# Kernel tuning notes

Hardware: AMD Instinct MI355X
Metric: run time of the kernel (lower is better)

## Reference

```python
import jax, jax.numpy as jnp
import numpy as np

NY = NX = 256
NT = 256
B = 2
NSRC = 2
NREC = 64
DY = DX = 5.0
DT = 5e-4
PML = 20
PML_FREQ = 25.0


def setup_inputs() -> dict:
    key = jax.random.key(0)
    k1, k2, k3, k4, k5, k6 = jax.random.split(key, 6)
    # physically plausible elastic model
    vp = 3000.0 + 200.0 * jax.random.uniform(k1, (NY, NX), dtype=jnp.float32)
    vs = 1500.0 + 100.0 * jax.random.uniform(k2, (NY, NX), dtype=jnp.float32)
    rho = 2200.0 + 100.0 * jax.random.uniform(k3, (NY, NX), dtype=jnp.float32)
    lamb = rho * (vp ** 2 - 2.0 * vs ** 2)
    mu = rho * vs ** 2
    buoyancy = 1.0 / rho
    source_amplitudes_y = 1e3 * jax.random.normal(k4, (B, NSRC, NT), dtype=jnp.float32)
    lo, hi = PML + 10, NY - PML - 10  # keep sources/receivers inside the PML
    source_locations_y = jax.random.randint(k5, (B, NSRC, 2), lo, hi)
    receiver_locations_y = jax.random.randint(k6, (B, NREC, 2), lo, hi)
    return {
        "lamb": lamb,
        "mu": mu,
        "buoyancy": buoyancy,
        "source_amplitudes_y": source_amplitudes_y,
        "source_locations_y": source_locations_y,
        "receiver_locations_y": receiver_locations_y,
    }


def _pml_coeffs(n, width, dx, dt, max_vel, freq):
    # C-PML coefficients a, b along one axis; zero outside the PML region.
    i = jnp.arange(n, dtype=jnp.float32)
    frac = jnp.maximum(
        jnp.clip((width - i) / width, 0.0, 1.0),
        jnp.clip((i - (n - 1 - width)) / width, 0.0, 1.0),
    )
    sigma_max = 3.0 * max_vel * np.log(1000.0) / (2.0 * width * dx)
    sigma = sigma_max * frac ** 2
    alpha = np.pi * freq * (1.0 - frac)
    b = jnp.exp(-(sigma + alpha) * dt)
    a = sigma / (sigma + alpha + 1e-9) * (b - 1.0)
    return a, b


# staggered 2nd-order forward/backward differences (zero beyond the edge)
def _dfy(f):
    return jnp.pad(f[:, 1:] - f[:, :-1], ((0, 0), (0, 1), (0, 0))) / DY

def _dby(f):
    return jnp.pad(f[:, 1:] - f[:, :-1], ((0, 0), (1, 0), (0, 0))) / DY

def _dfx(f):
    return jnp.pad(f[:, :, 1:] - f[:, :, :-1], ((0, 0), (0, 0), (0, 1))) / DX

def _dbx(f):
    return jnp.pad(f[:, :, 1:] - f[:, :, :-1], ((0, 0), (0, 0), (1, 0))) / DX


def _forward(lamb, mu, buoyancy, amps, src_loc, rec_loc):
    ny, nx = lamb.shape
    bsz, nsrc, nt = amps.shape
    max_vel = jax.lax.stop_gradient(jnp.sqrt((lamb + 2.0 * mu) * buoyancy).max())
    ay, by = _pml_coeffs(ny, PML, DY, DT, max_vel, PML_FREQ)
    ax, bx = _pml_coeffs(nx, PML, DX, DT, max_vel, PML_FREQ)
    ay, by = ay[None, :, None], by[None, :, None]
    ax, bx = ax[None, None, :], bx[None, None, :]
    sb = jnp.arange(bsz)[:, None]
    sy, sx = src_loc[..., 0], src_loc[..., 1]
    ry, rx = rec_loc[..., 0], rec_loc[..., 1]
    src_scale = DT * buoyancy[sy, sx]  # [B, nsrc]
    l2m = lamb + 2.0 * mu
    z = jnp.zeros((bsz, ny, nx), lamb.dtype)
    fields0 = (z,) * 13  # vy, vx, syy, sxy, sxx + 8 PML memory fields

    def step(carry, amp_t):
        (vy, vx, syy, sxy, sxx,
         m_syyy, m_sxyx, m_sxyy, m_sxxx,
         m_vyy, m_vxx, m_vyx, m_vxy) = carry
        # velocity updates (with PML memory on stress derivatives)
        d = _dby(syy); m_syyy = by * m_syyy + ay * d; d_syy_y = d + m_syyy
        d = _dbx(sxy); m_sxyx = bx * m_sxyx + ax * d; d_sxy_x = d + m_sxyx
        vy = vy + DT * buoyancy * (d_syy_y + d_sxy_x)
        d = _dfy(sxy); m_sxyy = by * m_sxyy + ay * d; d_sxy_y = d + m_sxyy
        d = _dfx(sxx); m_sxxx = bx * m_sxxx + ax * d; d_sxx_x = d + m_sxxx
        vx = vx + DT * buoyancy * (d_sxy_y + d_sxx_x)
        # y-oriented source injection into vy
        vy = vy.at[sb, sy, sx].add(amp_t * src_scale)
        # stress updates (with PML memory on velocity derivatives)
        d = _dfy(vy); m_vyy = by * m_vyy + ay * d; d_vy_y = d + m_vyy
        d = _dbx(vx); m_vxx = bx * m_vxx + ax * d; d_vx_x = d + m_vxx
        syy = syy + DT * (l2m * d_vy_y + lamb * d_vx_x)
        sxx = sxx + DT * (lamb * d_vy_y + l2m * d_vx_x)
        d = _dbx(vy); m_vyx = bx * m_vyx + ax * d; d_vy_x = d + m_vyx
        d = _dby(vx); m_vxy = by * m_vxy + ay * d; d_vx_y = d + m_vxy
        sxy = sxy + DT * mu * (d_vy_x + d_vx_y)
        rec = vy[sb, ry, rx]  # [B, nrec]
        return (vy, vx, syy, sxy, sxx,
                m_syyy, m_sxyx, m_sxyy, m_sxxx,
                m_vyy, m_vxx, m_vyx, m_vxy), rec

    _, recs = jax.lax.scan(jax.checkpoint(step), fields0, jnp.transpose(amps, (2, 0, 1)))
    return jnp.transpose(recs, (1, 2, 0))  # [shot, receiver, time]


def reference(lamb, mu, buoyancy, source_amplitudes_y, source_locations_y, receiver_locations_y):
    return _forward(lamb, mu, buoyancy, source_amplitudes_y,
                    source_locations_y, receiver_locations_y)
```

## Files before the change

### kernel.cpp

```cpp
#include <hip/hip_runtime.h>

#define NXc 256
#define NTc 256
#define NBLK 128
#define DTv 0.0005f
#define INVD 0.2f

#define COEF_OFF 0
#define EX_OFF  1024
#define EX_BLK  2048

__device__ __forceinline__ unsigned long long tld(const unsigned long long* p) {
  return __hip_atomic_load(p, __ATOMIC_RELAXED, __HIP_MEMORY_SCOPE_AGENT);
}
__device__ __forceinline__ void tst(unsigned long long* p, float v, unsigned tag) {
  unsigned long long u = ((unsigned long long)tag << 32) | (unsigned long long)__float_as_uint(v);
  __hip_atomic_store(p, u, __ATOMIC_RELAXED, __HIP_MEMORY_SCOPE_AGENT);
}
#define TVAL(x) __uint_as_float((unsigned)(x))
#define TTAG(x) ((unsigned)((x) >> 32))

__device__ __forceinline__ void bar_lds() {
  asm volatile("s_waitcnt lgkmcnt(0)" ::: "memory");
  __builtin_amdgcn_s_barrier();
  asm volatile("" ::: "memory");
}

__global__ __launch_bounds__(256) void setup_kernel(
    const float* __restrict__ lamb, const float* __restrict__ mu,
    const float* __restrict__ buoy, float* __restrict__ coef)
{
  __shared__ float red[256];
  const int tid = threadIdx.x;
  float m = 0.0f;
  for (int i = tid; i < 256*256; i += 256)
    m = fmaxf(m, sqrtf((lamb[i] + 2.0f*mu[i]) * buoy[i]));
  red[tid] = m;
  __syncthreads();
  for (int s = 128; s > 0; s >>= 1) {
    if (tid < s) red[tid] = fmaxf(red[tid], red[tid+s]);
    __syncthreads();
  }
  const float maxv = red[0];
  const float i_f = (float)tid;
  const float w = 20.0f;
  float f1 = fminf(fmaxf((w - i_f) * (1.0f/w), 0.0f), 1.0f);
  float f2 = fminf(fmaxf((i_f - (256.0f - 1.0f - w)) * (1.0f/w), 0.0f), 1.0f);
  float frac = fmaxf(f1, f2);
  float sigma_max = 3.0f * maxv * 6.907755278982137f / (2.0f * w * 5.0f);
  float sigma = sigma_max * frac * frac;
  float alpha = 3.14159265358979323f * 25.0f * (1.0f - frac);
  float bc = expf(-(sigma + alpha) * 0.0005f);
  float ac = sigma / (sigma + alpha + 1e-9f) * (bc - 1.0f);
  coef[tid]       = ac;
  coef[256 + tid] = bc;
  coef[512 + tid] = ac;
  coef[768 + tid] = bc;
}

__global__ __launch_bounds__(256) void elastic_col(
    const float* __restrict__ lamb_g, const float* __restrict__ mu_g,
    const float* __restrict__ buoy_g, const float* __restrict__ amps,
    const int* __restrict__ src_loc, const int* __restrict__ rec_loc,
    float* __restrict__ ws, float* __restrict__ out)
{
  __shared__ float SxyB[4][6], SxxB[4][6], VyB[4][4], VxB[4][4];

  const int blk = blockIdx.x;
  const int b = blk >> 6, bi = blk & 63;
  const int tx = threadIdx.x;
  const int lane = tx & 63, wv = tx >> 6;
  const int lo = bi << 2;
  const bool hasUp = bi > 0, hasDn = bi < 63;
  const bool xm_ok = tx > 0, xp_ok = tx < 255;

  const float* coef = ws + COEF_OFF;
  unsigned long long* exb = (unsigned long long*)(ws + EX_OFF);

  const float axv = coef[512+tx], bxv = coef[768+tx];

  float vy[6], vx[6], myy[6], myx[6], mxyy[6], mxx[6];
  float cay[6], cby[6], vdtb[6];
  #pragma unroll
  for (int r = 0; r < 6; ++r) {
    const int gy = lo - 1 + r;
    const bool ok = (gy >= 0) && (gy < 256);
    const int gc = ok ? gy : 0;
    vdtb[r] = ok ? DTv * buoy_g[gc*NXc + tx] : 0.f;
    cay[r]  = ok ? coef[gc] : 0.f;
    cby[r]  = ok ? coef[256+gc] : 1.f;
    vy[r]=vx[r]=myy[r]=myx[r]=mxyy[r]=mxx[r]=0.f;
  }
  float syy[4], sxy[4], sxx[4], mvyy[4], mvxx[4], mvyx[4], mvxy[4];
  float slam[4], smu[4], sl2m[4];
  #pragma unroll
  for (int j = 0; j < 4; ++j) {
    const int gy = lo + j;
    slam[j] = lamb_g[gy*NXc+tx]; smu[j] = mu_g[gy*NXc+tx];
    sl2m[j] = slam[j] + 2.f*smu[j];
    syy[j]=sxy[j]=sxx[j]=mvyy[j]=mvxx[j]=mvyx[j]=mvxy[j]=0.f;
  }

  int sk0=-1, sk1=-1, so0=0, so1=0;
  for (int i = 0; i < 4; ++i) {
    const int sb = i >> 1, sy = src_loc[2*i], sx = src_loc[2*i+1];
    if (sb == b && sx == tx) {
      const int r = sy - (lo - 1);
      if (r >= 0 && r < 6) { if (sk0 < 0) { sk0=r; so0=i*NTc; } else { sk1=r; so1=i*NTc; } }
    }
  }
  unsigned long long rL0=0,rH0=0,rL1=0,rH1=0,rL2=0,rH2=0,rL3=0,rH3=0;
  for (int i = 0; i < 128; ++i) {
    const int rb = i >> 6, ry = rec_loc[2*i], rx = rec_loc[2*i+1];
    if (rb == b && rx == tx) {
      const unsigned long long bit = 1ull << (i & 63);
      if (ry == lo)   { if (i<64) rL0|=bit; else rH0|=bit; }
      if (ry == lo+1) { if (i<64) rL1|=bit; else rH1|=bit; }
      if (ry == lo+2) { if (i<64) rL2|=bit; else rH2|=bit; }
      if (ry == lo+3) { if (i<64) rL3|=bit; else rH3|=bit; }
    }
  }
  const bool anyrec = (rL0|rH0|rL1|rH1|rL2|rH2|rL3|rH3) != 0ull;

  if (tx < 4*6) { SxyB[tx/6][tx%6]=0.f; SxxB[tx/6][tx%6]=0.f; }
  if (tx < 4*4) { VyB[tx/4][tx%4]=0.f;  VxB[tx/4][tx%4]=0.f; }
  __syncthreads();

  for (int t = 0; t < NTc; ++t) {
    float a0=0.f, a1=0.f;
    if (sk0>=0) a0 = amps[so0+t];
    if (sk1>=0) a1 = amps[so1+t];

    unsigned long long uw0=0,uw1=0,uw2=0,uw3=0, dw0=0,dw1=0,dw2=0,dw3=0;
    if (t > 0) {
      const size_t ps = (size_t)((t-1)&1)*NBLK;
      const unsigned long long* up = exb + (ps + (hasUp?blk-1:blk))*EX_BLK + tx;
      const unsigned long long* dn = exb + (ps + (hasDn?blk+1:blk))*EX_BLK + tx;
      const unsigned want = (unsigned)t;
      for (;;) {
        if (hasUp) { uw0=tld(up+4*256); uw1=tld(up+5*256); uw2=tld(up+6*256); uw3=tld(up+7*256); }
        if (hasDn) { dw0=tld(dn+0*256); dw1=tld(dn+1*256); dw2=tld(dn+2*256); dw3=tld(dn+3*256); }
        bool ok = true;
        if (hasUp) ok = ok && TTAG(uw0)==want && TTAG(uw1)==want && TTAG(uw2)==want && TTAG(uw3)==want;
        if (hasDn) ok = ok && TTAG(dw0)==want && TTAG(dw1)==want && TTAG(dw2)==want && TTAG(dw3)==want;
        if (ok) break;
      }
    }
    const float syyU2=TVAL(uw0), syyU1=TVAL(uw1), sxyU1=TVAL(uw2), sxxU1=TVAL(uw3);
    const float syyD =TVAL(dw0), sxyD4=TVAL(dw1), sxyD5=TVAL(dw2), sxxD =TVAL(dw3);

    if (lane == 63) { SxyB[wv][0]=sxyU1; SxyB[wv][5]=sxyD4; }
    if (lane == 0)  { SxxB[wv][0]=sxxU1; SxxB[wv][5]=sxxD; }
    bar_lds();

    {
      const float syE[7]  = {syyU2, syyU1, syy[0],syy[1],syy[2],syy[3], syyD};
      const float sxyE[6] = {sxyU1, sxy[0],sxy[1],sxy[2],sxy[3], sxyD4};
      const float sxxE[6] = {sxxU1, sxx[0],sxx[1],sxx[2],sxx[3], sxxD};
      #pragma unroll
      for (int r = 0; r < 6; ++r) {
        float sxym = __shfl_up(sxyE[r], 1, 64);
        if (lane == 0 && wv > 0) sxym = SxyB[wv-1][r];
        float sxxp = __shfl_down(sxxE[r], 1, 64);
        if (lane == 63 && wv < 3) sxxp = SxxB[wv+1][r];
        if (r == 0 && !hasUp) continue;
        if (r == 5 && !hasDn) continue;
        const int gy = lo - 1 + r;
        float d, u1, u2, u3, u4;
        d = (gy > 0) ? (syE[r+1] - syE[r]) * INVD : 0.f;
        myy[r] = cby[r]*myy[r] + cay[r]*d; u1 = d + myy[r];
        d = xm_ok ? (sxyE[r] - sxym) * INVD : 0.f;
        myx[r] = bxv*myx[r] + axv*d; u2 = d + myx[r];
        vy[r] += vdtb[r]*(u1+u2);
        float dfy;
        if (r < 5) dfy = (gy < 255) ? (sxyE[r+1] - sxyE[r]) * INVD : 0.f;
        else       dfy = (sxyD5 - sxyD4) * INVD;
        mxyy[r] = cby[r]*mxyy[r] + cay[r]*dfy; u3 = dfy + mxyy[r];
        d = xp_ok ? (sxxp - sxxE[r]) * INVD : 0.f;
        mxx[r] = bxv*mxx[r] + axv*d; u4 = d + mxx[r];
        vx[r] += vdtb[r]*(u3+u4);
        if (r == sk0) vy[r] += a0*vdtb[r];
        if (r == sk1) vy[r] += a1*vdtb[r];
      }
    }
    if (lane == 63) {
      VyB[wv][0]=vy[1]; VyB[wv][1]=vy[2]; VyB[wv][2]=vy[3]; VyB[wv][3]=vy[4];
      VxB[wv][0]=vx[1]; VxB[wv][1]=vx[2]; VxB[wv][2]=vx[3]; VxB[wv][3]=vx[4];
    }
    bar_lds();

    if (anyrec) {
      unsigned long long m;
      m=rL0; while(m){int i=__ffsll((long long)m)-1;m&=m-1;out[i*NTc+t]=vy[1];}
      m=rH0; while(m){int i=__ffsll((long long)m)-1;m&=m-1;out[(i+64)*NTc+t]=vy[1];}
      m=rL1; while(m){int i=__ffsll((long long)m)-1;m&=m-1;out[i*NTc+t]=vy[2];}
      m=rH1; while(m){int i=__ffsll((long long)m)-1;m&=m-1;out[(i+64)*NTc+t]=vy[2];}
      m=rL2; while(m){int i=__ffsll((long long)m)-1;m&=m-1;out[i*NTc+t]=vy[3];}
      m=rH2; while(m){int i=__ffsll((long long)m)-1;m&=m-1;out[(i+64)*NTc+t]=vy[3];}
      m=rL3; while(m){int i=__ffsll((long long)m)-1;m&=m-1;out[i*NTc+t]=vy[4];}
      m=rH3; while(m){int i=__ffsll((long long)m)-1;m&=m-1;out[(i+64)*NTc+t]=vy[4];}
    }

    {
      float vym[4], vxm[4];
      #pragma unroll
      for (int j = 0; j < 4; ++j) {
        vym[j] = __shfl_up(vy[j+1], 1, 64);
        vxm[j] = __shfl_up(vx[j+1], 1, 64);
        if (lane == 0 && wv > 0) { vym[j] = VyB[wv-1][j]; vxm[j] = VxB[wv-1][j]; }
      }
      #pragma unroll
      for (int j = 0; j < 4; ++j) {
        const int gy = lo + j;
        float d, u5, u6, u7, u8;
        d = (gy < 255) ? (vy[j+2] - vy[j+1]) * INVD : 0.f;
        mvyy[j] = cby[j+1]*mvyy[j] + cay[j+1]*d; u5 = d + mvyy[j];
        d = xm_ok ? (vx[j+1] - vxm[j]) * INVD : 0.f;
        mvxx[j] = bxv*mvxx[j] + axv*d; u6 = d + mvxx[j];
        syy[j] += DTv*(sl2m[j]*u5 + slam[j]*u6);
        sxx[j] += DTv*(slam[j]*u5 + sl2m[j]*u6);
        d = xm_ok ? (vy[j+1] - vym[j]) * INVD : 0.f;
        mvyx[j] = bxv*mvyx[j] + axv*d; u7 = d + mvyx[j];
        d = (gy > 0) ? (vx[j+1] - vx[j]) * INVD : 0.f;
        mvxy[j] = cby[j+1]*mvxy[j] + cay[j+1]*d; u8 = d + mvxy[j];
        sxy[j] += DTv*smu[j]*(u7+u8);
      }
    }

    {
      unsigned long long* Q = exb + ((size_t)(t&1)*NBLK + blk)*EX_BLK + tx;
      const unsigned wt = (unsigned)(t+1);
      tst(Q+0*256, syy[0], wt); tst(Q+1*256, sxy[0], wt);
      tst(Q+2*256, sxy[1], wt); tst(Q+3*256, sxx[0], wt);
      tst(Q+4*256, syy[2], wt); tst(Q+5*256, syy[3], wt);
      tst(Q+6*256, sxy[3], wt); tst(Q+7*256, sxx[3], wt);
    }
    if (lane == 63) { SxyB[wv][1]=sxy[0]; SxyB[wv][2]=sxy[1]; SxyB[wv][3]=sxy[2]; SxyB[wv][4]=sxy[3]; }
    if (lane == 0)  { SxxB[wv][1]=sxx[0]; SxxB[wv][2]=sxx[1]; SxxB[wv][3]=sxx[2]; SxxB[wv][4]=sxx[3]; }
  }
}

extern "C" void kernel_launch(void* const* d_in, const int* in_sizes, int n_in,
                              void* d_out, int out_size, void* d_ws, size_t ws_size,
                              hipStream_t stream) {
  const float* lamb    = (const float*)d_in[0];
  const float* mu      = (const float*)d_in[1];
  const float* buoy    = (const float*)d_in[2];
  const float* amps    = (const float*)d_in[3];
  const int*   src_loc = (const int*)d_in[4];
  const int*   rec_loc = (const int*)d_in[5];
  float* out = (float*)d_out;
  float* ws  = (float*)d_ws;

  hipMemsetAsync((char*)ws + EX_OFF*sizeof(float), 0,
                 (size_t)2*NBLK*EX_BLK*sizeof(unsigned long long), stream);

  hipLaunchKernelGGL(setup_kernel, dim3(1), dim3(256), 0, stream,
                     lamb, mu, buoy, ws + COEF_OFF);

  void* args[] = { (void*)&lamb, (void*)&mu, (void*)&buoy, (void*)&amps,
                   (void*)&src_loc, (void*)&rec_loc, (void*)&ws, (void*)&out };
  hipLaunchCooperativeKernel((void*)elastic_col, dim3(NBLK), dim3(256),
                             args, 0, stream);
}
```

Measured before the change: 787.0 us.

## Split domain into 256 two-row blocks with full-stress halo exchange

Each block now owns 2 rows instead of 4, doubling the grid to 256 cooperative blocks so more CUs share the per-step serial work. Neighbours publish all six stress values per column, and each block recomputes the halo velocity rows itself from those values instead of receiving them. Edge lanes also read the adjacent column's halo entries directly from global memory. The cost is more flag-polling traffic per step and duplicated halo velocity work relative to the useful work per block.

```diff
diff --git a/kernel.cpp b/kernel.cpp
--- a/kernel.cpp
+++ b/kernel.cpp
@@ -2,13 +2,14 @@
 
 #define NXc 256
 #define NTc 256
-#define NBLK 128
+#define NBLK 256
 #define DTv 0.0005f
 #define INVD 0.2f
 
 #define COEF_OFF 0
 #define EX_OFF  1024
-#define EX_BLK  2048
+#define EX_ENT  6
+#define EX_BLK  (EX_ENT*256)
 
 __device__ __forceinline__ unsigned long long tld(const unsigned long long* p) {
   return __hip_atomic_load(p, __ATOMIC_RELAXED, __HIP_MEMORY_SCOPE_AGENT);
@@ -58,20 +59,20 @@
   coef[768 + tid] = bc;
 }
 
-__global__ __launch_bounds__(256) void elastic_col(
+__global__ __launch_bounds__(256) void elastic_n2(
     const float* __restrict__ lamb_g, const float* __restrict__ mu_g,
     const float* __restrict__ buoy_g, const float* __restrict__ amps,
     const int* __restrict__ src_loc, const int* __restrict__ rec_loc,
     float* __restrict__ ws, float* __restrict__ out)
 {
-  __shared__ float SxyB[4][6], SxxB[4][6], VyB[4][4], VxB[4][4];
+  __shared__ float SxyB[4][2], SxxB[4][2], VyB[4][2], VxB[4][2];
 
   const int blk = blockIdx.x;
-  const int b = blk >> 6, bi = blk & 63;
+  const int b = blk >> 7, n = blk & 127;
   const int tx = threadIdx.x;
   const int lane = tx & 63, wv = tx >> 6;
-  const int lo = bi << 2;
-  const bool hasUp = bi > 0, hasDn = bi < 63;
+  const int lo = n << 1;
+  const bool hasUp = n > 0, hasDn = n < 127;
   const bool xm_ok = tx > 0, xp_ok = tx < 255;
 
   const float* coef = ws + COEF_OFF;
@@ -79,51 +80,48 @@
 
   const float axv = coef[512+tx], bxv = coef[768+tx];
 
-  float vy[6], vx[6], myy[6], myx[6], mxyy[6], mxx[6];
-  float cay[6], cby[6], vdtb[6];
-  #pragma unroll
-  for (int r = 0; r < 6; ++r) {
-    const int gy = lo - 1 + r;
-    const bool ok = (gy >= 0) && (gy < 256);
-    const int gc = ok ? gy : 0;
-    vdtb[r] = ok ? DTv * buoy_g[gc*NXc + tx] : 0.f;
-    cay[r]  = ok ? coef[gc] : 0.f;
-    cby[r]  = ok ? coef[256+gc] : 1.f;
-    vy[r]=vx[r]=myy[r]=myx[r]=mxyy[r]=mxx[r]=0.f;
-  }
-  float syy[4], sxy[4], sxx[4], mvyy[4], mvxx[4], mvyx[4], mvxy[4];
-  float slam[4], smu[4], sl2m[4];
-  #pragma unroll
-  for (int j = 0; j < 4; ++j) {
-    const int gy = lo + j;
-    slam[j] = lamb_g[gy*NXc+tx]; smu[j] = mu_g[gy*NXc+tx];
-    sl2m[j] = slam[j] + 2.f*smu[j];
-    syy[j]=sxy[j]=sxx[j]=mvyy[j]=mvxx[j]=mvyx[j]=mvxy[j]=0.f;
-  }
+  const float ayU = hasUp ? coef[lo-1] : 0.f;
+  const float byU = hasUp ? coef[256+lo-1] : 1.f;
+  const float dtbU = hasUp ? DTv*buoy_g[(lo-1)*NXc+tx] : 0.f;
+  const float ay0 = coef[lo],   by0 = coef[256+lo];
+  const float dtb0 = DTv*buoy_g[lo*NXc+tx];
+  const float ay1 = coef[lo+1], by1 = coef[256+lo+1];
+  const float dtb1 = DTv*buoy_g[(lo+1)*NXc+tx];
+  const float ayD = hasDn ? coef[lo+2] : 0.f;
+  const float byD = hasDn ? coef[256+lo+2] : 1.f;
+  const float dtbD = hasDn ? DTv*buoy_g[(lo+2)*NXc+tx] : 0.f;
+  const float lam0 = lamb_g[lo*NXc+tx],     mu0 = mu_g[lo*NXc+tx],     l2m0 = lam0+2.f*mu0;
+  const float lam1 = lamb_g[(lo+1)*NXc+tx], mu1 = mu_g[(lo+1)*NXc+tx], l2m1 = lam1+2.f*mu1;
+
+  float vy0=0,vy1=0,vx0=0,vx1=0, vyU=0,vxU=0, vyD=0,vxD=0;
+  float myy0=0,myy1=0,myx0=0,myx1=0,mxyy0=0,mxyy1=0,mxx0=0,mxx1=0;
+  float myyU=0,myxU=0,mxyyU=0,mxxU=0, myyD=0,myxD=0,mxyyD=0,mxxD=0;
+  float syy0=0,syy1=0,sxy0=0,sxy1=0,sxx0=0,sxx1=0;
+  float mvyy0=0,mvyy1=0,mvxx0=0,mvxx1=0,mvyx0=0,mvyx1=0,mvxy0=0,mvxy1=0;
 
   int sk0=-1, sk1=-1, so0=0, so1=0;
   for (int i = 0; i < 4; ++i) {
     const int sb = i >> 1, sy = src_loc[2*i], sx = src_loc[2*i+1];
     if (sb == b && sx == tx) {
       const int r = sy - (lo - 1);
-      if (r >= 0 && r < 6) { if (sk0 < 0) { sk0=r; so0=i*NTc; } else { sk1=r; so1=i*NTc; } }
-    }
-  }
-  unsigned long long rL0=0,rH0=0,rL1=0,rH1=0,rL2=0,rH2=0,rL3=0,rH3=0;
+      if (r >= 0 && r < 4) { if (sk0 < 0) { sk0=r; so0=i*NTc; } else { sk1=r; so1=i*NTc; } }
+    }
+  }
+  unsigned long long rA0=0,rA1=0,rB0=0,rB1=0;
   for (int i = 0; i < 128; ++i) {
     const int rb = i >> 6, ry = rec_loc[2*i], rx = rec_loc[2*i+1];
     if (rb == b && rx == tx) {
       const unsigned long long bit = 1ull << (i & 63);
-      if (ry == lo)   { if (i<64) rL0|=bit; else rH0|=bit; }
-      if (ry == lo+1) { if (i<64) rL1|=bit; else rH1|=bit; }
-      if (ry == lo+2) { if (i<64) rL2|=bit; else rH2|=bit; }
-      if (ry == lo+3) { if (i<64) rL3|=bit; else rH3|=bit; }
-    }
-  }
-  const bool anyrec = (rL0|rH0|rL1|rH1|rL2|rH2|rL3|rH3) != 0ull;
-
-  if (tx < 4*6) { SxyB[tx/6][tx%6]=0.f; SxxB[tx/6][tx%6]=0.f; }
-  if (tx < 4*4) { VyB[tx/4][tx%4]=0.f;  VxB[tx/4][tx%4]=0.f; }
+      if (ry == lo)   { if (i<64) rA0|=bit; else rA1|=bit; }
+      if (ry == lo+1) { if (i<64) rB0|=bit; else rB1|=bit; }
+    }
+  }
+  const bool recA = (rA0|rA1)!=0ull, recB = (rB0|rB1)!=0ull;
+
+  if (tx < 8) {
+    SxyB[tx>>1][tx&1]=0.f; SxxB[tx>>1][tx&1]=0.f;
+    VyB[tx>>1][tx&1]=0.f;  VxB[tx>>1][tx&1]=0.f;
+  }
   __syncthreads();
 
   for (int t = 0; t < NTc; ++t) {
@@ -131,112 +129,154 @@
     if (sk0>=0) a0 = amps[so0+t];
     if (sk1>=0) a1 = amps[so1+t];
 
-    unsigned long long uw0=0,uw1=0,uw2=0,uw3=0, dw0=0,dw1=0,dw2=0,dw3=0;
-    if (t > 0) {
-      const size_t ps = (size_t)((t-1)&1)*NBLK;
-      const unsigned long long* up = exb + (ps + (hasUp?blk-1:blk))*EX_BLK + tx;
-      const unsigned long long* dn = exb + (ps + (hasDn?blk+1:blk))*EX_BLK + tx;
-      const unsigned want = (unsigned)t;
-      for (;;) {
-        if (hasUp) { uw0=tld(up+4*256); uw1=tld(up+5*256); uw2=tld(up+6*256); uw3=tld(up+7*256); }
-        if (hasDn) { dw0=tld(dn+0*256); dw1=tld(dn+1*256); dw2=tld(dn+2*256); dw3=tld(dn+3*256); }
-        bool ok = true;
-        if (hasUp) ok = ok && TTAG(uw0)==want && TTAG(uw1)==want && TTAG(uw2)==want && TTAG(uw3)==want;
-        if (hasDn) ok = ok && TTAG(dw0)==want && TTAG(dw1)==want && TTAG(dw2)==want && TTAG(dw3)==want;
-        if (ok) break;
+    const size_t ps = (size_t)((t+1)&1)*NBLK;
+    const unsigned long long* up = exb + (ps + (size_t)(hasUp?blk-1:blk))*EX_BLK + tx;
+    const unsigned long long* dn = exb + (ps + (size_t)(hasDn?blk+1:blk))*EX_BLK + tx;
+    const unsigned want = (unsigned)t;
+    unsigned long long u0=0,u1=0,u3=0,u5=0,u3m=0,u5p=0;
+    unsigned long long d0=0,d2=0,d3=0,d4=0,d2m=0,d4p=0;
+    for (;;) {
+      bool ok = true;
+      if (hasUp) {
+        u0=tld(up+0*256); u1=tld(up+1*256); u3=tld(up+3*256); u5=tld(up+5*256);
+        ok = ok && TTAG(u0)==want && TTAG(u1)==want && TTAG(u3)==want && TTAG(u5)==want;
+        if (lane==0 && xm_ok)  { u3m=tld(up+3*256-1); ok = ok && TTAG(u3m)==want; }
+        if (lane==63 && xp_ok) { u5p=tld(up+5*256+1); ok = ok && TTAG(u5p)==want; }
       }
-    }
-    const float syyU2=TVAL(uw0), syyU1=TVAL(uw1), sxyU1=TVAL(uw2), sxxU1=TVAL(uw3);
-    const float syyD =TVAL(dw0), sxyD4=TVAL(dw1), sxyD5=TVAL(dw2), sxxD =TVAL(dw3);
-
-    if (lane == 63) { SxyB[wv][0]=sxyU1; SxyB[wv][5]=sxyD4; }
-    if (lane == 0)  { SxxB[wv][0]=sxxU1; SxxB[wv][5]=sxxD; }
+      if (hasDn) {
+        d0=tld(dn+0*256); d2=tld(dn+2*256); d3=tld(dn+3*256); d4=tld(dn+4*256);
+        ok = ok && TTAG(d0)==want && TTAG(d2)==want && TTAG(d3)==want && TTAG(d4)==want;
+        if (lane==0 && xm_ok)  { d2m=tld(dn+2*256-1); ok = ok && TTAG(d2m)==want; }
+        if (lane==63 && xp_ok) { d4p=tld(dn+4*256+1); ok = ok && TTAG(d4p)==want; }
+      }
+      if (ok) break;
+    }
+    const float syyU0=TVAL(u0), syyU1=TVAL(u1), sxyU1=TVAL(u3), sxxU1=TVAL(u5);
+    const float syyD0=TVAL(d0), sxyD0=TVAL(d2), sxyD1=TVAL(d3), sxxD0=TVAL(d4);
+    const float sxyU1m=TVAL(u3m), sxxU1p=TVAL(u5p);
+    const float sxyD0m=TVAL(d2m), sxxD0p=TVAL(d4p);
+
+    if (hasUp) {
+      float d,t1,t2,t3,t4;
+      d = (syyU1 - syyU0) * INVD;
+      myyU = byU*myyU + ayU*d; t1 = d + myyU;
+      float sm = __shfl_up(sxyU1, 1, 64); if (lane==0) sm = sxyU1m;
+      d = xm_ok ? (sxyU1 - sm) * INVD : 0.f;
+      myxU = bxv*myxU + axv*d; t2 = d + myxU;
+      vyU += dtbU*(t1+t2);
+      d = (sxy0 - sxyU1) * INVD;
+      mxyyU = byU*mxyyU + ayU*d; t3 = d + mxyyU;
+      float sp = __shfl_down(sxxU1, 1, 64); if (lane==63) sp = sxxU1p;
+      d = xp_ok ? (sp - sxxU1) * INVD : 0.f;
+      mxxU = bxv*mxxU + axv*d; t4 = d + mxxU;
+      vxU += dtbU*(t3+t4);
+      if (sk0==0) vyU += a0*dtbU;
+      if (sk1==0) vyU += a1*dtbU;
+    }
+    {
+      float d,t1,t2,t3,t4;
+      d = hasUp ? (syy0 - syyU1) * INVD : 0.f;
+      myy0 = by0*myy0 + ay0*d; t1 = d + myy0;
+      float sm = __shfl_up(sxy0, 1, 64); if (lane==0 && wv>0) sm = SxyB[wv-1][0];
+      d = xm_ok ? (sxy0 - sm) * INVD : 0.f;
+      myx0 = bxv*myx0 + axv*d; t2 = d + myx0;
+      vy0 += dtb0*(t1+t2);
+      d = (sxy1 - sxy0) * INVD;
+      mxyy0 = by0*mxyy0 + ay0*d; t3 = d + mxyy0;
+      float sp = __shfl_down(sxx0, 1, 64); if (lane==63 && wv<3) sp = SxxB[wv+1][0];
+      d = xp_ok ? (sp - sxx0) * INVD : 0.f;
+      mxx0 = bxv*mxx0 + axv*d; t4 = d + mxx0;
+      vx0 += dtb0*(t3+t4);
+      if (sk0==1) vy0 += a0*dtb0;
+      if (sk1==1) vy0 += a1*dtb0;
+    }
+    {
+      float d,t1,t2,t3,t4;
+      d = (syy1 - syy0) * INVD;
+      myy1 = by1*myy1 + ay1*d; t1 = d + myy1;
+      float sm = __shfl_up(sxy1, 1, 64); if (lane==0 && wv>0) sm = SxyB[wv-1][1];
+      d = xm_ok ? (sxy1 - sm) * INVD : 0.f;
+      myx1 = bxv*myx1 + axv*d; t2 = d + myx1;
+      vy1 += dtb1*(t1+t2);
+      d = hasDn ? (sxyD0 - sxy1) * INVD : 0.f;
+      mxyy1 = by1*mxyy1 + ay1*d; t3 = d + mxyy1;
+      float sp = __shfl_down(sxx1, 1, 64); if (lane==63 && wv<3) sp = SxxB[wv+1][1];
+      d = xp_ok ? (sp - sxx1) * INVD : 0.f;
+      mxx1 = bxv*mxx1 + axv*d; t4 = d + mxx1;
+      vx1 += dtb1*(t3+t4);
+      if (sk0==2) vy1 += a0*dtb1;
+      if (sk1==2) vy1 += a1*dtb1;
+    }
+    if (hasDn) {
+      float d,t1,t2,t3,t4;
+      d = (syyD0 - syy1) * INVD;
+      myyD = byD*myyD + ayD*d; t1 = d + myyD;
+      float sm = __shfl_up(sxyD0, 1, 64); if (lane==0) sm = sxyD0m;
+      d = xm_ok ? (sxyD0 - sm) * INVD : 0.f;
+      myxD = bxv*myxD + axv*d; t2 = d + myxD;
+      vyD += dtbD*(t1+t2);
+      d = (sxyD1 - sxyD0) * INVD;
+      mxyyD = byD*mxyyD + ayD*d; t3 = d + mxyyD;
+      float sp = __shfl_down(sxxD0, 1, 64); if (lane==63) sp = sxxD0p;
+      d = xp_ok ? (sp - sxxD0) * INVD : 0.f;
+      mxxD = bxv*mxxD + axv*d; t4 = d + mxxD;
+      vxD += dtbD*(t3+t4);
+      if (sk0==3) vyD += a0*dtbD;
+      if (sk1==3) vyD += a1*dtbD;
+    }
+
+    if (lane == 63) { VyB[wv][0]=vy0; VyB[wv][1]=vy1; VxB[wv][0]=vx0; VxB[wv][1]=vx1; }
+    if (recA) {
+      unsigned long long m;
+      m=rA0; while(m){int i=__ffsll((long long)m)-1;m&=m-1;out[i*NTc+t]=vy0;}
+      m=rA1; while(m){int i=__ffsll((long long)m)-1;m&=m-1;out[(i+64)*NTc+t]=vy0;}
+    }
+    if (recB) {
+      unsigned long long m;
+      m=rB0; while(m){int i=__ffsll((long long)m)-1;m&=m-1;out[i*NTc+t]=vy1;}
+      m=rB1; while(m){int i=__ffsll((long long)m)-1;m&=m-1;out[(i+64)*NTc+t]=vy1;}
+    }
     bar_lds();
 
+    unsigned long long* Q = exb + ((size_t)(t&1)*NBLK + blk)*EX_BLK + tx;
+    const unsigned wt = (unsigned)(t+1);
     {
-      const float syE[7]  = {syyU2, syyU1, syy[0],syy[1],syy[2],syy[3], syyD};
-      const float sxyE[6] = {sxyU1, sxy[0],sxy[1],sxy[2],sxy[3], sxyD4};
-      const float sxxE[6] = {sxxU1, sxx[0],sxx[1],sxx[2],sxx[3], sxxD};
-      #pragma unroll
-      for (int r = 0; r < 6; ++r) {
-        float sxym = __shfl_up(sxyE[r], 1, 64);
-        if (lane == 0 && wv > 0) sxym = SxyB[wv-1][r];
-        float sxxp = __shfl_down(sxxE[r], 1, 64);
-        if (lane == 63 && wv < 3) sxxp = SxxB[wv+1][r];
-        if (r == 0 && !hasUp) continue;
-        if (r == 5 && !hasDn) continue;
-        const int gy = lo - 1 + r;
-        float d, u1, u2, u3, u4;
-        d = (gy > 0) ? (syE[r+1] - syE[r]) * INVD : 0.f;
-        myy[r] = cby[r]*myy[r] + cay[r]*d; u1 = d + myy[r];
-        d = xm_ok ? (sxyE[r] - sxym) * INVD : 0.f;
-        myx[r] = bxv*myx[r] + axv*d; u2 = d + myx[r];
-        vy[r] += vdtb[r]*(u1+u2);
-        float dfy;
-        if (r < 5) dfy = (gy < 255) ? (sxyE[r+1] - sxyE[r]) * INVD : 0.f;
-        else       dfy = (sxyD5 - sxyD4) * INVD;
-        mxyy[r] = cby[r]*mxyy[r] + cay[r]*dfy; u3 = dfy + mxyy[r];
-        d = xp_ok ? (sxxp - sxxE[r]) * INVD : 0.f;
-        mxx[r] = bxv*mxx[r] + axv*d; u4 = d + mxx[r];
-        vx[r] += vdtb[r]*(u3+u4);
-        if (r == sk0) vy[r] += a0*vdtb[r];
-        if (r == sk1) vy[r] += a1*vdtb[r];
-      }
-    }
-    if (lane == 63) {
-      VyB[wv][0]=vy[1]; VyB[wv][1]=vy[2]; VyB[wv][2]=vy[3]; VyB[wv][3]=vy[4];
-      VxB[wv][0]=vx[1]; VxB[wv][1]=vx[2]; VxB[wv][2]=vx[3]; VxB[wv][3]=vx[4];
-    }
+      float vym = __shfl_up(vy0, 1, 64); if (lane==0 && wv>0) vym = VyB[wv-1][0];
+      float vxm = __shfl_up(vx0, 1, 64); if (lane==0 && wv>0) vxm = VxB[wv-1][0];
+      float d,u5,u6,u7,u8;
+      d = (vy1 - vy0) * INVD;
+      mvyy0 = by0*mvyy0 + ay0*d; u5 = d + mvyy0;
+      d = xm_ok ? (vx0 - vxm) * INVD : 0.f;
+      mvxx0 = bxv*mvxx0 + axv*d; u6 = d + mvxx0;
+      syy0 += DTv*(l2m0*u5 + lam0*u6);
+      sxx0 += DTv*(lam0*u5 + l2m0*u6);
+      d = xm_ok ? (vy0 - vym) * INVD : 0.f;
+      mvyx0 = bxv*mvyx0 + axv*d; u7 = d + mvyx0;
+      d = hasUp ? (vx0 - vxU) * INVD : 0.f;
+      mvxy0 = by0*mvxy0 + ay0*d; u8 = d + mvxy0;
+      sxy0 += DTv*mu0*(u7+u8);
+      tst(Q+0*256, syy0, wt); tst(Q+2*256, sxy0, wt); tst(Q+4*256, sxx0, wt);
+    }
+    {
+      float vym = __shfl_up(vy1, 1, 64); if (lane==0 && wv>0) vym = VyB[wv-1][1];
+      float vxm = __shfl_up(vx1, 1, 64); if (lane==0 && wv>0) vxm = VxB[wv-1][1];
+      float d,u5,u6,u7,u8;
+      d = hasDn ? (vyD - vy1) * INVD : 0.f;
+      mvyy1 = by1*mvyy1 + ay1*d; u5 = d + mvyy1;
+      d = xm_ok ? (vx1 - vxm) * INVD : 0.f;
+      mvxx1 = bxv*mvxx1 + axv*d; u6 = d + mvxx1;
+      syy1 += DTv*(l2m1*u5 + lam1*u6);
+      sxx1 += DTv*(lam1*u5 + l2m1*u6);
+      d = xm_ok ? (vy1 - vym) * INVD : 0.f;
+      mvyx1 = bxv*mvyx1 + axv*d; u7 = d + mvyx1;
+      d = (vx1 - vx0) * INVD;
+      mvxy1 = by1*mvxy1 + ay1*d; u8 = d + mvxy1;
+      sxy1 += DTv*mu1*(u7+u8);
+      tst(Q+1*256, syy1, wt); tst(Q+3*256, sxy1, wt); tst(Q+5*256, sxx1, wt);
+    }
+    if (lane == 63) { SxyB[wv][0]=sxy0; SxyB[wv][1]=sxy1; }
+    if (lane == 0)  { SxxB[wv][0]=sxx0; SxxB[wv][1]=sxx1; }
     bar_lds();
-
-    if (anyrec) {
-      unsigned long long m;
-      m=rL0; while(m){int i=__ffsll((long long)m)-1;m&=m-1;out[i*NTc+t]=vy[1];}
-      m=rH0; while(m){int i=__ffsll((long long)m)-1;m&=m-1;out[(i+64)*NTc+t]=vy[1];}
-      m=rL1; while(m){int i=__ffsll((long long)m)-1;m&=m-1;out[i*NTc+t]=vy[2];}
-      m=rH1; while(m){int i=__ffsll((long long)m)-1;m&=m-1;out[(i+64)*NTc+t]=vy[2];}
-      m=rL2; while(m){int i=__ffsll((long long)m)-1;m&=m-1;out[i*NTc+t]=vy[3];}
-      m=rH2; while(m){int i=__ffsll((long long)m)-1;m&=m-1;out[(i+64)*NTc+t]=vy[3];}
-      m=rL3; while(m){int i=__ffsll((long long)m)-1;m&=m-1;out[i*NTc+t]=vy[4];}
-      m=rH3; while(m){int i=__ffsll((long long)m)-1;m&=m-1;out[(i+64)*NTc+t]=vy[4];}
-    }
-
-    {
-      float vym[4], vxm[4];
-      #pragma unroll
-      for (int j = 0; j < 4; ++j) {
-        vym[j] = __shfl_up(vy[j+1], 1, 64);
-        vxm[j] = __shfl_up(vx[j+1], 1, 64);
-        if (lane == 0 && wv > 0) { vym[j] = VyB[wv-1][j]; vxm[j] = VxB[wv-1][j]; }
-      }
-      #pragma unroll
-      for (int j = 0; j < 4; ++j) {
-        const int gy = lo + j;
-        float d, u5, u6, u7, u8;
-        d = (gy < 255) ? (vy[j+2] - vy[j+1]) * INVD : 0.f;
-        mvyy[j] = cby[j+1]*mvyy[j] + cay[j+1]*d; u5 = d + mvyy[j];
-        d = xm_ok ? (vx[j+1] - vxm[j]) * INVD : 0.f;
-        mvxx[j] = bxv*mvxx[j] + axv*d; u6 = d + mvxx[j];
-        syy[j] += DTv*(sl2m[j]*u5 + slam[j]*u6);
-        sxx[j] += DTv*(slam[j]*u5 + sl2m[j]*u6);
-        d = xm_ok ? (vy[j+1] - vym[j]) * INVD : 0.f;
-        mvyx[j] = bxv*mvyx[j] + axv*d; u7 = d + mvyx[j];
-        d = (gy > 0) ? (vx[j+1] - vx[j]) * INVD : 0.f;
-        mvxy[j] = cby[j+1]*mvxy[j] + cay[j+1]*d; u8 = d + mvxy[j];
-        sxy[j] += DTv*smu[j]*(u7+u8);
-      }
-    }
-
-    {
-      unsigned long long* Q = exb + ((size_t)(t&1)*NBLK + blk)*EX_BLK + tx;
-      const unsigned wt = (unsigned)(t+1);
-      tst(Q+0*256, syy[0], wt); tst(Q+1*256, sxy[0], wt);
-      tst(Q+2*256, sxy[1], wt); tst(Q+3*256, sxx[0], wt);
-      tst(Q+4*256, syy[2], wt); tst(Q+5*256, syy[3], wt);
-      tst(Q+6*256, sxy[3], wt); tst(Q+7*256, sxx[3], wt);
-    }
-    if (lane == 63) { SxyB[wv][1]=sxy[0]; SxyB[wv][2]=sxy[1]; SxyB[wv][3]=sxy[2]; SxyB[wv][4]=sxy[3]; }
-    if (lane == 0)  { SxxB[wv][1]=sxx[0]; SxxB[wv][2]=sxx[1]; SxxB[wv][3]=sxx[2]; SxxB[wv][4]=sxx[3]; }
   }
 }
 
@@ -260,6 +300,6 @@
 
   void* args[] = { (void*)&lamb, (void*)&mu, (void*)&buoy, (void*)&amps,
                    (void*)&src_loc, (void*)&rec_loc, (void*)&ws, (void*)&out };
-  hipLaunchCooperativeKernel((void*)elastic_col, dim3(NBLK), dim3(256),
+  hipLaunchCooperativeKernel((void*)elastic_n2, dim3(NBLK), dim3(256),
                              args, 0, stream);
 }
```

After: 868.9 us. 10.4% more time.

## Use 8-row strips per 1024-thread block with LDS-resident fields and interior-first updates

Applied to the files above, without the earlier changes.

Each block now owns 8 grid rows per shot (64 blocks of 1024 threads) instead of 4 rows (128 blocks of 256 threads). Stress and velocity rows live in shared memory, replacing the wave shuffles and boundary buffers. Interior velocity rows are updated before polling neighbour halos, so the spin-wait overlaps with useful work. Only two waves poll the halo flags, and the last step skips publishing. The cost is half as many blocks and a larger LDS footprint, and each block does more work per step on the serial dependency chain.

```diff
diff --git a/kernel.cpp b/kernel.cpp
--- a/kernel.cpp
+++ b/kernel.cpp
@@ -2,7 +2,7 @@
 
 #define NXc 256
 #define NTc 256
-#define NBLK 128
+#define NBLK 64
 #define DTv 0.0005f
 #define INVD 0.2f
 
@@ -58,185 +58,210 @@
   coef[768 + tid] = bc;
 }
 
-__global__ __launch_bounds__(256) void elastic_col(
+#define VUPD(k, syA, syB, sxyC, sxyCm, sxyD, sxxC, sxxCp, upok, dnok)      \
+  { float d_, t1_, t2_, t3_, t4_;                                          \
+    d_ = (upok) ? ((syB) - (syA))*INVD : 0.f;                              \
+    myy_[k] = vby[k]*myy_[k] + vay[k]*d_; t1_ = d_ + myy_[k];              \
+    d_ = xm_ok ? ((sxyC) - (sxyCm))*INVD : 0.f;                            \
+    myx_[k] = bxv*myx_[k] + axv*d_; t2_ = d_ + myx_[k];                    \
+    d_ = (dnok) ? ((sxyD) - (sxyC))*INVD : 0.f;                            \
+    mxyy_[k] = vby[k]*mxyy_[k] + vay[k]*d_; t3_ = d_ + mxyy_[k];           \
+    d_ = xp_ok ? ((sxxCp) - (sxxC))*INVD : 0.f;                            \
+    mxx_[k] = bxv*mxx_[k] + axv*d_; t4_ = d_ + mxx_[k];                    \
+    vy_[k] += vdtb[k]*(t1_+t2_);                                           \
+    vx_[k] += vdtb[k]*(t3_+t4_);                                           \
+    if ((k) == sk0) vy_[k] += a0*vdtb[k];                                  \
+    if ((k) == sk1) vy_[k] += a1*vdtb[k];                                  \
+    V[0][ty + 4*(k)][tx] = vy_[k]; V[1][ty + 4*(k)][tx] = vx_[k]; }
+
+#define VINT(k, r) VUPD(k, S[0][(r)-1][tx], S[0][r][tx], S[1][r][tx],      \
+                        S[1][r][txm], S[1][(r)+1][tx], S[2][r][tx],        \
+                        S[2][r][txp], true, true)
+
+#define SUPD(j, rs)                                                        \
+  { float d_, u5_, u6_, u7_, u8_; const int gy_ = lo + (rs);               \
+    d_ = (gy_ < 255) ? (V[0][(rs)+2][tx]-V[0][(rs)+1][tx])*INVD : 0.f;     \
+    mvyy_[j] = sby[j]*mvyy_[j] + say[j]*d_; u5_ = d_ + mvyy_[j];           \
+    d_ = xm_ok ? (V[1][(rs)+1][tx]-V[1][(rs)+1][txm])*INVD : 0.f;          \
+    mvxx_[j] = bxv*mvxx_[j] + axv*d_; u6_ = d_ + mvxx_[j];                 \
+    syy_[j] += DTv*(sl2m[j]*u5_ + slam[j]*u6_);                            \
+    sxx_[j] += DTv*(slam[j]*u5_ + sl2m[j]*u6_);                            \
+    d_ = xm_ok ? (V[0][(rs)+1][tx]-V[0][(rs)+1][txm])*INVD : 0.f;          \
+    mvyx_[j] = bxv*mvyx_[j] + axv*d_; u7_ = d_ + mvyx_[j];                 \
+    d_ = (gy_ > 0) ? (V[1][(rs)+1][tx]-V[1][(rs)][tx])*INVD : 0.f;         \
+    mvxy_[j] = sby[j]*mvxy_[j] + say[j]*d_; u8_ = d_ + mvxy_[j];           \
+    sxy_[j] += DTv*smu[j]*(u7_+u8_);                                       \
+    S[0][rs][tx]=syy_[j]; S[1][rs][tx]=sxy_[j]; S[2][rs][tx]=sxx_[j]; }
+
+__global__ __launch_bounds__(1024) void elastic_w8(
     const float* __restrict__ lamb_g, const float* __restrict__ mu_g,
     const float* __restrict__ buoy_g, const float* __restrict__ amps,
     const int* __restrict__ src_loc, const int* __restrict__ rec_loc,
     float* __restrict__ ws, float* __restrict__ out)
 {
-  __shared__ float SxyB[4][6], SxxB[4][6], VyB[4][4], VxB[4][4];
+  __shared__ float S[3][8][NXc];
+  __shared__ float V[2][10][NXc];
 
   const int blk = blockIdx.x;
-  const int b = blk >> 6, bi = blk & 63;
-  const int tx = threadIdx.x;
-  const int lane = tx & 63, wv = tx >> 6;
-  const int lo = bi << 2;
-  const bool hasUp = bi > 0, hasDn = bi < 63;
+  const int b = blk >> 5, n = blk & 31;
+  const int tid = threadIdx.x;
+  const int ty = tid >> 8, tx = tid & 255;
+  const int lo = n << 3;
+  const bool hasUp = n > 0, hasDn = n < 31;
+  const int txm = tx ? tx-1 : 0;
+  const int txp = (tx < 255) ? tx+1 : 255;
   const bool xm_ok = tx > 0, xp_ok = tx < 255;
 
   const float* coef = ws + COEF_OFF;
   unsigned long long* exb = (unsigned long long*)(ws + EX_OFF);
-
   const float axv = coef[512+tx], bxv = coef[768+tx];
 
-  float vy[6], vx[6], myy[6], myx[6], mxyy[6], mxx[6];
-  float cay[6], cby[6], vdtb[6];
+  float vy_[3], vx_[3], myy_[3], myx_[3], mxyy_[3], mxx_[3];
+  float vay[3], vby[3], vdtb[3];
   #pragma unroll
-  for (int r = 0; r < 6; ++r) {
-    const int gy = lo - 1 + r;
-    const bool ok = (gy >= 0) && (gy < 256);
+  for (int k = 0; k < 3; ++k) {
+    const int rr = ty + 4*k;
+    const int gy = lo + rr - 1;
+    const bool ok = (rr < 10) && (gy >= 0) && (gy < 256);
     const int gc = ok ? gy : 0;
-    vdtb[r] = ok ? DTv * buoy_g[gc*NXc + tx] : 0.f;
-    cay[r]  = ok ? coef[gc] : 0.f;
-    cby[r]  = ok ? coef[256+gc] : 1.f;
-    vy[r]=vx[r]=myy[r]=myx[r]=mxyy[r]=mxx[r]=0.f;
-  }
-  float syy[4], sxy[4], sxx[4], mvyy[4], mvxx[4], mvyx[4], mvxy[4];
-  float slam[4], smu[4], sl2m[4];
+    vdtb[k] = ok ? DTv*buoy_g[gc*NXc+tx] : 0.f;
+    vay[k] = ok ? coef[gc] : 0.f;
+    vby[k] = ok ? coef[256+gc] : 1.f;
+    vy_[k]=vx_[k]=myy_[k]=myx_[k]=mxyy_[k]=mxx_[k]=0.f;
+  }
+  float syy_[2], sxy_[2], sxx_[2], mvyy_[2], mvxx_[2], mvyx_[2], mvxy_[2];
+  float slam[2], smu[2], sl2m[2], say[2], sby[2];
   #pragma unroll
-  for (int j = 0; j < 4; ++j) {
-    const int gy = lo + j;
+  for (int j = 0; j < 2; ++j) {
+    const int gy = lo + ty + 4*j;
     slam[j] = lamb_g[gy*NXc+tx]; smu[j] = mu_g[gy*NXc+tx];
-    sl2m[j] = slam[j] + 2.f*smu[j];
-    syy[j]=sxy[j]=sxx[j]=mvyy[j]=mvxx[j]=mvyx[j]=mvxy[j]=0.f;
+    sl2m[j] = slam[j]+2.f*smu[j];
+    say[j] = coef[gy]; sby[j] = coef[256+gy];
+    syy_[j]=sxy_[j]=sxx_[j]=mvyy_[j]=mvxx_[j]=mvyx_[j]=mvxy_[j]=0.f;
   }
 
   int sk0=-1, sk1=-1, so0=0, so1=0;
   for (int i = 0; i < 4; ++i) {
-    const int sb = i >> 1, sy = src_loc[2*i], sx = src_loc[2*i+1];
+    const int sb = i>>1, sy = src_loc[2*i], sx = src_loc[2*i+1];
     if (sb == b && sx == tx) {
-      const int r = sy - (lo - 1);
-      if (r >= 0 && r < 6) { if (sk0 < 0) { sk0=r; so0=i*NTc; } else { sk1=r; so1=i*NTc; } }
-    }
-  }
-  unsigned long long rL0=0,rH0=0,rL1=0,rH1=0,rL2=0,rH2=0,rL3=0,rH3=0;
+      const int rr = sy - lo + 1;
+      if (rr >= 0 && rr < 10 && (rr & 3) == ty) {
+        const int k = rr >> 2;
+        if (sk0 < 0) { sk0=k; so0=i*NTc; } else { sk1=k; so1=i*NTc; }
+      }
+    }
+  }
+  const int gyA = lo + ((ty==0)?3:(ty==1)?0:(ty==2)?1:2);
+  const int gyB = lo + ((ty==0)?7:(ty==1)?4:(ty==2)?5:6);
+  unsigned long long mA0=0,mA1=0,mB0=0,mB1=0;
   for (int i = 0; i < 128; ++i) {
-    const int rb = i >> 6, ry = rec_loc[2*i], rx = rec_loc[2*i+1];
-    if (rb == b && rx == tx) {
-      const unsigned long long bit = 1ull << (i & 63);
-      if (ry == lo)   { if (i<64) rL0|=bit; else rH0|=bit; }
-      if (ry == lo+1) { if (i<64) rL1|=bit; else rH1|=bit; }
-      if (ry == lo+2) { if (i<64) rL2|=bit; else rH2|=bit; }
-      if (ry == lo+3) { if (i<64) rL3|=bit; else rH3|=bit; }
-    }
-  }
-  const bool anyrec = (rL0|rH0|rL1|rH1|rL2|rH2|rL3|rH3) != 0ull;
-
-  if (tx < 4*6) { SxyB[tx/6][tx%6]=0.f; SxxB[tx/6][tx%6]=0.f; }
-  if (tx < 4*4) { VyB[tx/4][tx%4]=0.f;  VxB[tx/4][tx%4]=0.f; }
+    const int rb=i>>6, ry=rec_loc[2*i], rx=rec_loc[2*i+1];
+    if (rb==b && rx==tx) {
+      const unsigned long long bit = 1ull << (i&63);
+      if (ry==gyA) { if (i<64) mA0|=bit; else mA1|=bit; }
+      if (ry==gyB) { if (i<64) mB0|=bit; else mB1|=bit; }
+    }
+  }
+  const bool recA=(mA0|mA1)!=0ull, recB=(mB0|mB1)!=0ull;
+
+  { float* p=&S[0][0][0]; for(int i=tid;i<3*8*NXc;i+=1024) p[i]=0.f;
+    float* q=&V[0][0][0]; for(int i=tid;i<2*10*NXc;i+=1024) q[i]=0.f; }
   __syncthreads();
 
   for (int t = 0; t < NTc; ++t) {
     float a0=0.f, a1=0.f;
-    if (sk0>=0) a0 = amps[so0+t];
-    if (sk1>=0) a1 = amps[so1+t];
-
-    unsigned long long uw0=0,uw1=0,uw2=0,uw3=0, dw0=0,dw1=0,dw2=0,dw3=0;
-    if (t > 0) {
+    if (sk0>=0) a0=amps[so0+t];
+    if (sk1>=0) a1=amps[so1+t];
+
+    if (ty==0)      { VINT(1,3) }
+    else if (ty==1) { VINT(1,4) }
+    else if (ty==2) { VINT(0,1) VINT(1,5) }
+    else            { VINT(0,2) VINT(1,6) }
+
+    unsigned long long w4=0,w5=0,w6=0,w6m=0,w7=0,w7p=0;
+    unsigned long long z0=0,z1=0,z1m=0,z2=0,z3=0,z3p=0;
+    if (t > 0 && ty < 2) {
       const size_t ps = (size_t)((t-1)&1)*NBLK;
-      const unsigned long long* up = exb + (ps + (hasUp?blk-1:blk))*EX_BLK + tx;
-      const unsigned long long* dn = exb + (ps + (hasDn?blk+1:blk))*EX_BLK + tx;
+      const unsigned long long* up = exb + (ps + (size_t)(hasUp?blk-1:blk))*EX_BLK;
+      const unsigned long long* dn = exb + (ps + (size_t)(hasDn?blk+1:blk))*EX_BLK;
       const unsigned want = (unsigned)t;
-      for (;;) {
-        if (hasUp) { uw0=tld(up+4*256); uw1=tld(up+5*256); uw2=tld(up+6*256); uw3=tld(up+7*256); }
-        if (hasDn) { dw0=tld(dn+0*256); dw1=tld(dn+1*256); dw2=tld(dn+2*256); dw3=tld(dn+3*256); }
-        bool ok = true;
-        if (hasUp) ok = ok && TTAG(uw0)==want && TTAG(uw1)==want && TTAG(uw2)==want && TTAG(uw3)==want;
-        if (hasDn) ok = ok && TTAG(dw0)==want && TTAG(dw1)==want && TTAG(dw2)==want && TTAG(dw3)==want;
-        if (ok) break;
-      }
-    }
-    const float syyU2=TVAL(uw0), syyU1=TVAL(uw1), sxyU1=TVAL(uw2), sxxU1=TVAL(uw3);
-    const float syyD =TVAL(dw0), sxyD4=TVAL(dw1), sxyD5=TVAL(dw2), sxxD =TVAL(dw3);
-
-    if (lane == 63) { SxyB[wv][0]=sxyU1; SxyB[wv][5]=sxyD4; }
-    if (lane == 0)  { SxxB[wv][0]=sxxU1; SxxB[wv][5]=sxxD; }
+      if (ty == 0) {
+        for (;;) {
+          bool ok = true;
+          if (hasUp) {
+            w4=tld(up+4*256+tx); w5=tld(up+5*256+tx); w6=tld(up+6*256+tx);
+            w6m=tld(up+6*256+txm); w7=tld(up+7*256+tx); w7p=tld(up+7*256+txp);
+            ok = ok && TTAG(w4)==want && TTAG(w5)==want && TTAG(w6)==want &&
+                 TTAG(w6m)==want && TTAG(w7)==want && TTAG(w7p)==want;
+          }
+          if (hasDn) { z1=tld(dn+1*256+tx); ok = ok && TTAG(z1)==want; }
+          if (ok) break;
+        }
+      } else {
+        for (;;) {
+          bool ok = true;
+          if (hasUp) { w5=tld(up+5*256+tx); ok = ok && TTAG(w5)==want; }
+          if (hasDn) {
+            z0=tld(dn+0*256+tx); z1=tld(dn+1*256+tx); z1m=tld(dn+1*256+txm);
+            z2=tld(dn+2*256+tx); z3=tld(dn+3*256+tx); z3p=tld(dn+3*256+txp);
+            ok = ok && TTAG(z0)==want && TTAG(z1)==want && TTAG(z1m)==want &&
+                 TTAG(z2)==want && TTAG(z3)==want && TTAG(z3p)==want;
+          }
+          if (ok) break;
+        }
+      }
+    }
+    asm volatile("" ::: "memory");
+
+    if (ty == 0) {
+      if (hasUp) {
+        VUPD(0, TVAL(w4), TVAL(w5), TVAL(w6), TVAL(w6m), S[1][0][tx],
+             TVAL(w7), TVAL(w7p), true, true)
+      }
+      VUPD(2, S[0][6][tx], S[0][7][tx], S[1][7][tx], S[1][7][txm],
+           TVAL(z1), S[2][7][tx], S[2][7][txp], true, hasDn)
+    } else if (ty == 1) {
+      VUPD(0, TVAL(w5), S[0][0][tx], S[1][0][tx], S[1][0][txm],
+           S[1][1][tx], S[2][0][tx], S[2][0][txp], hasUp, true)
+      if (hasDn) {
+        VUPD(2, S[0][7][tx], TVAL(z0), TVAL(z1), TVAL(z1m), TVAL(z2),
+             TVAL(z3), TVAL(z3p), true, true)
+      }
+    }
+
+    if (recA) {
+      const float v = (ty==0) ? vy_[1] : vy_[0];
+      unsigned long long m;
+      m=mA0; while(m){int i=__ffsll((long long)m)-1;m&=m-1;out[i*NTc+t]=v;}
+      m=mA1; while(m){int i=__ffsll((long long)m)-1;m&=m-1;out[(i+64)*NTc+t]=v;}
+    }
+    if (recB) {
+      const float v = (ty==0) ? vy_[2] : vy_[1];
+      unsigned long long m;
+      m=mB0; while(m){int i=__ffsll((long long)m)-1;m&=m-1;out[i*NTc+t]=v;}
+      m=mB1; while(m){int i=__ffsll((long long)m)-1;m&=m-1;out[(i+64)*NTc+t]=v;}
+    }
+
     bar_lds();
 
-    {
-      const float syE[7]  = {syyU2, syyU1, syy[0],syy[1],syy[2],syy[3], syyD};
-      const float sxyE[6] = {sxyU1, sxy[0],sxy[1],sxy[2],sxy[3], sxyD4};
-      const float sxxE[6] = {sxxU1, sxx[0],sxx[1],sxx[2],sxx[3], sxxD};
-      #pragma unroll
-      for (int r = 0; r < 6; ++r) {
-        float sxym = __shfl_up(sxyE[r], 1, 64);
-        if (lane == 0 && wv > 0) sxym = SxyB[wv-1][r];
-        float sxxp = __shfl_down(sxxE[r], 1, 64);
-        if (lane == 63 && wv < 3) sxxp = SxxB[wv+1][r];
-        if (r == 0 && !hasUp) continue;
-        if (r == 5 && !hasDn) continue;
-        const int gy = lo - 1 + r;
-        float d, u1, u2, u3, u4;
-        d = (gy > 0) ? (syE[r+1] - syE[r]) * INVD : 0.f;
-        myy[r] = cby[r]*myy[r] + cay[r]*d; u1 = d + myy[r];
-        d = xm_ok ? (sxyE[r] - sxym) * INVD : 0.f;
-        myx[r] = bxv*myx[r] + axv*d; u2 = d + myx[r];
-        vy[r] += vdtb[r]*(u1+u2);
-        float dfy;
-        if (r < 5) dfy = (gy < 255) ? (sxyE[r+1] - sxyE[r]) * INVD : 0.f;
-        else       dfy = (sxyD5 - sxyD4) * INVD;
-        mxyy[r] = cby[r]*mxyy[r] + cay[r]*dfy; u3 = dfy + mxyy[r];
-        d = xp_ok ? (sxxp - sxxE[r]) * INVD : 0.f;
-        mxx[r] = bxv*mxx[r] + axv*d; u4 = d + mxx[r];
-        vx[r] += vdtb[r]*(u3+u4);
-        if (r == sk0) vy[r] += a0*vdtb[r];
-        if (r == sk1) vy[r] += a1*vdtb[r];
-      }
-    }
-    if (lane == 63) {
-      VyB[wv][0]=vy[1]; VyB[wv][1]=vy[2]; VyB[wv][2]=vy[3]; VyB[wv][3]=vy[4];
-      VxB[wv][0]=vx[1]; VxB[wv][1]=vx[2]; VxB[wv][2]=vx[3]; VxB[wv][3]=vx[4];
+    unsigned long long* Q = exb + ((size_t)(t&1)*NBLK + blk)*EX_BLK + tx;
+    const unsigned wt = (unsigned)(t+1);
+    const bool doship = (t < NTc-1);
+    SUPD(0, ty)
+    if (ty == 0) {
+      if (doship) { tst(Q+0*256, syy_[0], wt); tst(Q+1*256, sxy_[0], wt);
+                    tst(Q+3*256, sxx_[0], wt); }
+    } else if (ty == 1) {
+      if (doship) { tst(Q+2*256, sxy_[0], wt); }
+    }
+    SUPD(1, ty+4)
+    if (ty == 2) {
+      if (doship) { tst(Q+4*256, syy_[1], wt); }
+    } else if (ty == 3) {
+      if (doship) { tst(Q+5*256, syy_[1], wt); tst(Q+6*256, sxy_[1], wt);
+                    tst(Q+7*256, sxx_[1], wt); }
     }
     bar_lds();
-
-    if (anyrec) {
-      unsigned long long m;
-      m=rL0; while(m){int i=__ffsll((long long)m)-1;m&=m-1;out[i*NTc+t]=vy[1];}
-      m=rH0; while(m){int i=__ffsll((long long)m)-1;m&=m-1;out[(i+64)*NTc+t]=vy[1];}
-      m=rL1; while(m){int i=__ffsll((long long)m)-1;m&=m-1;out[i*NTc+t]=vy[2];}
-      m=rH1; while(m){int i=__ffsll((long long)m)-1;m&=m-1;out[(i+64)*NTc+t]=vy[2];}
-      m=rL2; while(m){int i=__ffsll((long long)m)-1;m&=m-1;out[i*NTc+t]=vy[3];}
-      m=rH2; while(m){int i=__ffsll((long long)m)-1;m&=m-1;out[(i+64)*NTc+t]=vy[3];}
-      m=rL3; while(m){int i=__ffsll((long long)m)-1;m&=m-1;out[i*NTc+t]=vy[4];}
-      m=rH3; while(m){int i=__ffsll((long long)m)-1;m&=m-1;out[(i+64)*NTc+t]=vy[4];}
-    }
-
-    {
-      float vym[4], vxm[4];
-      #pragma unroll
-      for (int j = 0; j < 4; ++j) {
-        vym[j] = __shfl_up(vy[j+1], 1, 64);
-        vxm[j] = __shfl_up(vx[j+1], 1, 64);
-        if (lane == 0 && wv > 0) { vym[j] = VyB[wv-1][j]; vxm[j] = VxB[wv-1][j]; }
-      }
-      #pragma unroll
-      for (int j = 0; j < 4; ++j) {
-        const int gy = lo + j;
-        float d, u5, u6, u7, u8;
-        d = (gy < 255) ? (vy[j+2] - vy[j+1]) * INVD : 0.f;
-        mvyy[j] = cby[j+1]*mvyy[j] + cay[j+1]*d; u5 = d + mvyy[j];
-        d = xm_ok ? (vx[j+1] - vxm[j]) * INVD : 0.f;
-        mvxx[j] = bxv*mvxx[j] + axv*d; u6 = d + mvxx[j];
-        syy[j] += DTv*(sl2m[j]*u5 + slam[j]*u6);
-        sxx[j] += DTv*(slam[j]*u5 + sl2m[j]*u6);
-        d = xm_ok ? (vy[j+1] - vym[j]) * INVD : 0.f;
-        mvyx[j] = bxv*mvyx[j] + axv*d; u7 = d + mvyx[j];
-        d = (gy > 0) ? (vx[j+1] - vx[j]) * INVD : 0.f;
-        mvxy[j] = cby[j+1]*mvxy[j] + cay[j+1]*d; u8 = d + mvxy[j];
-        sxy[j] += DTv*smu[j]*(u7+u8);
-      }
-    }
-
-    {
-      unsigned long long* Q = exb + ((size_t)(t&1)*NBLK + blk)*EX_BLK + tx;
-      const unsigned wt = (unsigned)(t+1);
-      tst(Q+0*256, syy[0], wt); tst(Q+1*256, sxy[0], wt);
-      tst(Q+2*256, sxy[1], wt); tst(Q+3*256, sxx[0], wt);
-      tst(Q+4*256, syy[2], wt); tst(Q+5*256, syy[3], wt);
-      tst(Q+6*256, sxy[3], wt); tst(Q+7*256, sxx[3], wt);
-    }
-    if (lane == 63) { SxyB[wv][1]=sxy[0]; SxyB[wv][2]=sxy[1]; SxyB[wv][3]=sxy[2]; SxyB[wv][4]=sxy[3]; }
-    if (lane == 0)  { SxxB[wv][1]=sxx[0]; SxxB[wv][2]=sxx[1]; SxxB[wv][3]=sxx[2]; SxxB[wv][4]=sxx[3]; }
   }
 }
 
@@ -260,6 +285,6 @@
 
   void* args[] = { (void*)&lamb, (void*)&mu, (void*)&buoy, (void*)&amps,
                    (void*)&src_loc, (void*)&rec_loc, (void*)&ws, (void*)&out };
-  hipLaunchCooperativeKernel((void*)elastic_col, dim3(NBLK), dim3(256),
+  hipLaunchCooperativeKernel((void*)elastic_w8, dim3(NBLK), dim3(1024),
                              args, 0, stream);
 }
```

After: 1.184 ms. 50.4% more time.
